# Kernel optimization log

Hardware: AMD Instinct MI355X
Metric: run time of the kernel (lower is better)

## Reference

```python
import jax, jax.numpy as jnp
import numpy as np

VOCAB = 9
D = 128      # EMBED_DIM
S = 64       # SEQ_LEN / context_length
B = 512      # batch
NH = 4       # num_heads
DH = D // NH # head dim = 32
NB = 2       # num_blocks
EPS = 1e-5


def setup_inputs() -> dict:
    key = jax.random.key(0)
    ks = jax.random.split(key, 10)
    rn = lambda k, shape: jax.random.normal(k, shape, jnp.float32) * 0.02
    return {
        "x": jax.random.randint(ks[0], (B, S), 0, VOCAB),
        "emb": rn(ks[1], (VOCAB, D)),
        "ln1_w": jnp.ones((NB, D), jnp.float32),          # pre-sLSTM LayerNorm weight
        "Wg": rn(ks[2], (NB, 4, NH, DH, DH)),             # headwise gate projections (i,f,z,o)
        "R": rn(ks[3], (NB, NH, DH, 4 * DH)),             # recurrent kernels per head
        "bias": rn(ks[4], (NB, NH, 4, DH)),               # cell bias per head/gate
        "gn_w": jnp.ones((NB, D), jnp.float32),           # multi-head (group) norm weight
        "ln2_w": jnp.ones((NB, D), jnp.float32),          # pre-FF LayerNorm weight
        "ff_up_w": rn(ks[5], (NB, 2 * D, D)),             # gated FF up projection
        "ff_down_w": rn(ks[6], (NB, D, D)),               # FF down projection
        "post_w": jnp.ones((D,), jnp.float32),            # post-blocks LayerNorm weight
        "proj_w": rn(ks[7], (VOCAB, D)),
        "proj_b": jnp.zeros((VOCAB,), jnp.float32),
    }


def _layernorm(x, w):
    mu = x.mean(-1, keepdims=True)
    var = x.var(-1, keepdims=True)
    return (x - mu) * jax.lax.rsqrt(var + EPS) * w


def _mh_groupnorm(h, w):
    # h: [B,S,NH,DH] -> normalize over DH per head, scale by per-channel w [D]
    mu = h.mean(-1, keepdims=True)
    var = h.var(-1, keepdims=True)
    hn = (h - mu) * jax.lax.rsqrt(var + EPS)
    return hn.reshape(h.shape[0], h.shape[1], D) * w


def _slstm_layer(xh, Wg, R, b):
    # xh: [B,S,NH,DH]; Wg: [4,NH,DH,DH]; R: [NH,DH,4*DH]; b: [NH,4,DH]
    gx = jnp.einsum('bsnh,gnkh->sbngk', xh, Wg)  # [S,B,NH,4,DH] gate preacts (i,f,z,o)

    def step(carry, g):
        h, c, n, m = carry  # each [B,NH,DH]
        ry = jnp.einsum('bnh,nhk->bnk', h, R).reshape(h.shape[0], NH, 4, DH)
        raw = g + ry + b
        i_r, f_r, z_r, o_r = raw[:, :, 0], raw[:, :, 1], raw[:, :, 2], raw[:, :, 3]
        logfplusm = m + jax.nn.log_sigmoid(f_r)
        mnew = jnp.maximum(i_r, logfplusm)            # stabilizer
        ig = jnp.exp(i_r - mnew)
        fg = jnp.exp(logfplusm - mnew)
        cnew = fg * c + ig * jnp.tanh(z_r)
        nnew = fg * n + ig
        hnew = jax.nn.sigmoid(o_r) * cnew / nnew
        return (hnew, cnew, nnew, mnew), hnew

    z0 = jnp.zeros((xh.shape[0], NH, DH), xh.dtype)
    _, hs = jax.lax.scan(step, (z0, z0, z0, z0), gx)
    return hs.transpose(1, 0, 2, 3)  # [B,S,NH,DH]


def reference(x, emb, ln1_w, Wg, R, bias, gn_w, ln2_w, ff_up_w, ff_down_w, post_w, proj_w, proj_b):
    h = emb[x]  # [B,S,D]
    for bi in range(NB):
        xn = _layernorm(h, ln1_w[bi])
        y = _slstm_layer(xn.reshape(h.shape[0], S, NH, DH), Wg[bi], R[bi], bias[bi])
        h = h + _mh_groupnorm(y, gn_w[bi])
        xn = _layernorm(h, ln2_w[bi])
        up = xn @ ff_up_w[bi].T                       # [B,S,2D]
        gate, upv = up[..., :D], up[..., D:]
        h = h + (jax.nn.gelu(gate, approximate=False) * upv) @ ff_down_w[bi].T
    h = _layernorm(h, post_w)
    return h @ proj_w.T + proj_b  # [B,S,VOCAB]
```

## Files before the change

### kernel.cpp

```cpp
#include <hip/hip_runtime.h>
#include <math.h>

#define D      128
#define S_LEN  64
#define B_SZ   512
#define NH     4
#define DH     32
#define NB     2
#define VOCAB  9
#define EPS    1e-5f
#define NTOK   (B_SZ * S_LEN)

template <int CTRL>
__device__ __forceinline__ float dppf(float x) {
    return __int_as_float(__builtin_amdgcn_update_dpp(
        0, __float_as_int(x), CTRL, 0xF, 0xF, true));
}
__device__ __forceinline__ float wsum64(float x) {
    x += dppf<0x111>(x);
    x += dppf<0x112>(x);
    x += dppf<0x114>(x);
    x += dppf<0x118>(x);
    x += dppf<0x142>(x);
    x += dppf<0x143>(x);
    return __int_as_float(__builtin_amdgcn_readlane(__float_as_int(x), 63));
}

__device__ __forceinline__ int xc3(int t, int c) { return c ^ (((t >> 1) & 7) << 2); }
__device__ __forceinline__ int xa (int t, int c) { return c ^ ((t & 7) << 2); }
__device__ __forceinline__ int xg (int c)        { return c ^ ((c >> 5) << 3); }

__global__ __launch_bounds__(256) void k_embed(const int* __restrict__ x,
                                               const float* __restrict__ emb,
                                               float* __restrict__ h,
                                               float* __restrict__ stats)
{
    int lane = threadIdx.x & 63;
    int wv   = threadIdx.x >> 6;
    int tok  = blockIdx.x * 4 + wv;
    int xi   = x[tok];
    float2 v = ((const float2*)(emb + xi * D))[lane];
    ((float2*)(h + (size_t)tok * D))[lane] = v;
    float s1 = wsum64(v.x + v.y);
    float s2 = wsum64(v.x * v.x + v.y * v.y);
    float mu  = s1 * (1.0f / D);
    float var = s2 * (1.0f / D) - mu * mu;
    if (lane == 0) {
        stats[tok * 2]     = mu;
        stats[tok * 2 + 1] = rsqrtf(var + EPS);
    }
}

__global__ __launch_bounds__(256, 2) void k_gx(const float* __restrict__ Wg,
                                               const float* __restrict__ bias,
                                               const float* __restrict__ lnw,
                                               const float* __restrict__ h,
                                               const float* __restrict__ stats,
                                               float* __restrict__ gx)
{
    __shared__ float xs[32 * 128];
    __shared__ float wl[4 * 32 * 128];

    int tid  = threadIdx.x;
    int lane = tid & 63;
    int wv   = tid >> 6;
    size_t tok0 = (size_t)blockIdx.x * 32;

    {
        int q = tid & 7;
        #pragma unroll
        for (int it = 0; it < 16; ++it) {
            int row = it * 32 + (tid >> 3);
            int g  = row >> 7;
            int n  = (row >> 5) & 3;
            int hh = row & 31;
            float4 v = *(const float4*)(Wg + row * 32 + q * 4);
            int col = g * 32 + hh;
            int sw  = q << 2;
            float* dst = wl + n * 4096;
            dst[(q * 4 + 0) * 128 + (col ^ sw)] = v.x;
            dst[(q * 4 + 1) * 128 + (col ^ sw)] = v.y;
            dst[(q * 4 + 2) * 128 + (col ^ sw)] = v.z;
            dst[(q * 4 + 3) * 128 + (col ^ sw)] = v.w;
        }
    }
    for (int i = 0; i < 8; ++i) {
        int t = wv * 8 + i;
        const float* hp = h + (tok0 + t) * D;
        float mu = stats[(tok0 + t) * 2];
        float rs = stats[(tok0 + t) * 2 + 1];
        float v1 = (hp[lane]      - mu) * rs * lnw[lane];
        float v2 = (hp[64 + lane] - mu) * rs * lnw[64 + lane];
        xs[t * 128 + xg(lane)]      = v1;
        xs[t * 128 + xg(lane + 64)] = v2;
    }
    __syncthreads();

    int nh   = lane >> 4;
    int col0 = (lane & 15) * 8;
    int t0   = wv * 8;

    float acc[8][8];
    #pragma unroll
    for (int j = 0; j < 8; ++j)
        #pragma unroll
        for (int cc = 0; cc < 8; ++cc) acc[j][cc] = 0.f;

    const float* wbase = wl + nh * 4096;
    #pragma unroll 4
    for (int k = 0; k < 32; ++k) {
        int sw = (k >> 2) << 2;
        float4 w0 = *(const float4*)&wbase[k * 128 + (col0 ^ sw)];
        float4 w1 = *(const float4*)&wbase[k * 128 + ((col0 + 4) ^ sw)];
        int ac = (nh * 32 + k) ^ (nh << 3);
        #pragma unroll
        for (int j = 0; j < 8; ++j) {
            float a = xs[(t0 + j) * 128 + ac];
            acc[j][0] = fmaf(a, w0.x, acc[j][0]);
            acc[j][1] = fmaf(a, w0.y, acc[j][1]);
            acc[j][2] = fmaf(a, w0.z, acc[j][2]);
            acc[j][3] = fmaf(a, w0.w, acc[j][3]);
            acc[j][4] = fmaf(a, w1.x, acc[j][4]);
            acc[j][5] = fmaf(a, w1.y, acc[j][5]);
            acc[j][6] = fmaf(a, w1.z, acc[j][6]);
            acc[j][7] = fmaf(a, w1.w, acc[j][7]);
        }
    }

    float4 bb0 = *(const float4*)(bias + nh * 128 + col0);
    float4 bb1 = *(const float4*)(bias + nh * 128 + col0 + 4);
    #pragma unroll
    for (int j = 0; j < 8; ++j) {
        int gt = (int)tok0 + t0 + j;
        int bb = gt >> 6;
        int ss = gt & 63;
        float* op = gx + ((size_t)(bb * NH + nh) * S_LEN + ss) * 128 + col0;
        float4 o0v, o1v;
        o0v.x = acc[j][0] + bb0.x; o0v.y = acc[j][1] + bb0.y;
        o0v.z = acc[j][2] + bb0.z; o0v.w = acc[j][3] + bb0.w;
        o1v.x = acc[j][4] + bb1.x; o1v.y = acc[j][5] + bb1.y;
        o1v.z = acc[j][6] + bb1.z; o1v.w = acc[j][7] + bb1.w;
        *(float4*)op       = o0v;
        *(float4*)(op + 4) = o1v;
    }
}

__global__ __launch_bounds__(64, 1) void k_scan(const float* __restrict__ Rm,
                                                const float* __restrict__ gnw,
                                                const float* __restrict__ gx,
                                                float* __restrict__ h)
{
    __shared__ float WA[8][64][4];
    __shared__ float WB[8][64][4];

    int b    = blockIdx.x >> 2;
    int n    = blockIdx.x & 3;
    int lane = threadIdx.x;
    int e    = lane >> 1;
    int sub  = lane & 1;
    int colA = sub * DH + e;

    #pragma unroll
    for (int cc = 0; cc < 8; ++cc) {
        float4 a, bv;
        #pragma unroll
        for (int j = 0; j < 4; ++j) {
            ((float*)&a)[j]  = Rm[(n * DH + cc * 4 + j) * 128 + colA];
            ((float*)&bv)[j] = Rm[(n * DH + cc * 4 + j) * 128 + 64 + colA];
        }
        *(float4*)WA[cc][lane] = a;
        *(float4*)WB[cc][lane] = bv;
    }
    float gw = gnw[n * DH + e];
    __syncthreads();

    float c = 0.f, nacc = 0.f, m = 0.f;
    float hu[DH];
    #pragma unroll
    for (int i = 0; i < DH; ++i) hu[i] = 0.f;

    float* hb = h + ((size_t)b * S_LEN) * D + n * DH;
    const float* gxp = gx + ((size_t)(b * NH + n) * S_LEN) * 128;

    float pGA[4], pGB[4], pHR[4];
    #pragma unroll
    for (int k = 0; k < 4; ++k) {
        pGA[k] = gxp[k * 128 + colA];
        pGB[k] = gxp[k * 128 + 64 + colA];
        pHR[k] = hb[k * D + e];
    }

    #pragma unroll 4
    for (int s = 0; s < S_LEN; ++s) {
        int sp = (s + 4 < S_LEN) ? s + 4 : S_LEN - 1;
        float nGA = gxp[sp * 128 + colA];
        float nGB = gxp[sp * 128 + 64 + colA];
        float nHR = hb[sp * D + e];

        float r0=0,r1=0,r2=0,r3=0,q0=0,q1=0,q2=0,q3=0;
        #pragma unroll
        for (int cc = 0; cc < 8; ++cc) {
            float4 wa = *(const float4*)WA[cc][lane];
            float4 wb = *(const float4*)WB[cc][lane];
            r0 = fmaf(hu[cc*4+0], wa.x, r0);
            r1 = fmaf(hu[cc*4+1], wa.y, r1);
            r2 = fmaf(hu[cc*4+2], wa.z, r2);
            r3 = fmaf(hu[cc*4+3], wa.w, r3);
            q0 = fmaf(hu[cc*4+0], wb.x, q0);
            q1 = fmaf(hu[cc*4+1], wb.y, q1);
            q2 = fmaf(hu[cc*4+2], wb.z, q2);
            q3 = fmaf(hu[cc*4+3], wb.w, q3);
        }
        float rawA = pGA[0] + ((r0 + r1) + (r2 + r3));
        float rawB = pGB[0] + ((q0 + q1) + (q2 + q3));

        float xA = dppf<0xB1>(rawA);
        float xB = dppf<0xB1>(rawB);
        float i_r = sub ? xA   : rawA;
        float f_r = sub ? rawA : xA;
        float z_r = sub ? xB   : rawB;
        float o_r = sub ? rawB : xB;

        float lsf  = fminf(f_r, 0.f)
                   - 0.69314718055994531f * __log2f(1.0f + __expf(-fabsf(f_r)));
        float lfm  = m + lsf;
        float mnew = fmaxf(i_r, lfm);
        float ig   = __expf(i_r - mnew);
        float fg   = __expf(lfm - mnew);
        float t    = __expf(2.f * z_r);
        float tz   = 1.f - 2.f / (t + 1.f);
        c    = fg * c + ig * tz;
        nacc = fg * nacc + ig;
        m    = mnew;
        float hv = c / (nacc * (1.f + __expf(-o_r)));

        float s1 = wsum64(hv);
        float s2 = wsum64(hv * hv);
        float mu  = s1 * (1.f / 64.f);
        float var = s2 * (1.f / 64.f) - mu * mu;
        float hn  = (hv - mu) * rsqrtf(var + EPS) * gw;

        if (!sub) hb[s * D + e] = pHR[0] + hn;

        #pragma unroll
        for (int i = 0; i < DH; ++i)
            hu[i] = __int_as_float(
                __builtin_amdgcn_readlane(__float_as_int(hv), 2 * i));

        pGA[0]=pGA[1]; pGA[1]=pGA[2]; pGA[2]=pGA[3]; pGA[3]=nGA;
        pGB[0]=pGB[1]; pGB[1]=pGB[2]; pGB[2]=pGB[3]; pGB[3]=nGB;
        pHR[0]=pHR[1]; pHR[1]=pHR[2]; pHR[2]=pHR[3]; pHR[3]=nHR;
    }
}

template <int LAST>
__global__ __launch_bounds__(256, 2) void k_ff(float* __restrict__ h,
                                               const float* __restrict__ ln2w,
                                               const float* __restrict__ wup,
                                               const float* __restrict__ wdn,
                                               float* __restrict__ stats_out,
                                               const float* __restrict__ lastw,
                                               const float* __restrict__ projw,
                                               const float* __restrict__ projb,
                                               float* __restrict__ out)
{
    __shared__ float xs[32 * 128];
    __shared__ float as_[32 * 64];
    __shared__ float wt[2 * 32 * 64];

    int tid  = threadIdx.x;
    int lane = tid & 63;
    int wv   = tid >> 6;
    size_t tok0 = (size_t)blockIdx.x * 32;

    for (int i = 0; i < 8; ++i) {
        int t = wv * 8 + i;
        const float* hp = h + (tok0 + t) * D;
        float v1 = hp[lane], v2 = hp[64 + lane];
        float s1 = wsum64(v1 + v2);
        float s2 = wsum64(v1 * v1 + v2 * v2);
        float mu = s1 * (1.0f / D);
        float rs = rsqrtf(s2 * (1.0f / D) - mu * mu + EPS);
        xs[t * D + xc3(t, lane)]      = (v1 - mu) * rs * ln2w[lane];
        xs[t * D + xc3(t, lane + 64)] = (v2 - mu) * rs * ln2w[64 + lane];
    }

    int q     = tid & 7;
    int r0    = tid >> 3;
    int goff0 = r0 * D + q * 4;
    int goff1 = (r0 + 32) * D + q * 4;
    int s0    = r0 ^ (q << 2);
    int kb    = q * 4;

    auto ffld = [&](int id, float4* pre) {
        int p = (id >= 6) ? 1 : 0;
        int j = id - p * 6;
        const float* b0;
        const float* b1;
        if (j < 4) { b0 = wup + (p * 64) * D + j * 32;
                     b1 = wup + (128 + p * 64) * D + j * 32; }
        else       { int jj = j - 4;
                     b0 = wdn + p * 64 + jj * 32;
                     b1 = wdn + 64 * D + p * 64 + jj * 32; }
        pre[0] = *(const float4*)(b0 + goff0);
        pre[1] = *(const float4*)(b0 + goff1);
        pre[2] = *(const float4*)(b1 + goff0);
        pre[3] = *(const float4*)(b1 + goff1);
    };
    auto fst = [&](const float4* pre) {
        #pragma unroll
        for (int cc = 0; cc < 4; ++cc) {
            const float* p0 = (const float*)&pre[0];
            const float* p1 = (const float*)&pre[1];
            const float* p2 = (const float*)&pre[2];
            const float* p3 = (const float*)&pre[3];
            wt[(kb + cc) * 64 + s0]           = p0[cc];
            wt[(kb + cc) * 64 + s0 + 32]      = p1[cc];
            wt[2048 + (kb + cc) * 64 + s0]      = p2[cc];
            wt[2048 + (kb + cc) * 64 + s0 + 32] = p3[cc];
        }
    };

    int ti = tid >> 4;
    int oi = tid & 15;
    int t0 = ti * 2;
    int o0 = oi * 4;

    float accd[2][2][4];
    #pragma unroll
    for (int a1 = 0; a1 < 2; ++a1)
        #pragma unroll
        for (int j = 0; j < 2; ++j)
            #pragma unroll
            for (int cc = 0; cc < 4; ++cc) accd[a1][j][cc] = 0.f;

    float4 pre[4];
    ffld(0, pre);
    int id = 1;

    #pragma unroll
    for (int p = 0; p < 2; ++p) {
        float accg[2][4], accv[2][4];
        #pragma unroll
        for (int j = 0; j < 2; ++j)
            #pragma unroll
            for (int cc = 0; cc < 4; ++cc) { accg[j][cc] = 0.f; accv[j][cc] = 0.f; }

        for (int c4 = 0; c4 < 4; ++c4) {
            __syncthreads();
            fst(pre);
            if (id < 12) ffld(id, pre);
            ++id;
            __syncthreads();
            int kc = c4 * 32;
            #pragma unroll
            for (int k4 = 0; k4 < 8; ++k4) {
                float4 a0 = *(const float4*)&xs[t0 * D + xc3(t0, kc + k4 * 4)];
                float4 a1v = *(const float4*)&xs[(t0 + 1) * D + xc3(t0 + 1, kc + k4 * 4)];
                int ws = k4 << 2;
                #pragma unroll
                for (int i = 0; i < 4; ++i) {
                    int k = k4 * 4 + i;
                    float4 bg = *(const float4*)&wt[k * 64 + (o0 ^ ws)];
                    float4 bv = *(const float4*)&wt[2048 + k * 64 + (o0 ^ ws)];
                    float ax0 = ((const float*)&a0)[i];
                    float ax1 = ((const float*)&a1v)[i];
                    accg[0][0] = fmaf(ax0, bg.x, accg[0][0]);
                    accg[0][1] = fmaf(ax0, bg.y, accg[0][1]);
                    accg[0][2] = fmaf(ax0, bg.z, accg[0][2]);
                    accg[0][3] = fmaf(ax0, bg.w, accg[0][3]);
                    accg[1][0] = fmaf(ax1, bg.x, accg[1][0]);
                    accg[1][1] = fmaf(ax1, bg.y, accg[1][1]);
                    accg[1][2] = fmaf(ax1, bg.z, accg[1][2]);
                    accg[1][3] = fmaf(ax1, bg.w, accg[1][3]);
                    accv[0][0] = fmaf(ax0, bv.x, accv[0][0]);
                    accv[0][1] = fmaf(ax0, bv.y, accv[0][1]);
                    accv[0][2] = fmaf(ax0, bv.z, accv[0][2]);
                    accv[0][3] = fmaf(ax0, bv.w, accv[0][3]);
                    accv[1][0] = fmaf(ax1, bv.x, accv[1][0]);
                    accv[1][1] = fmaf(ax1, bv.y, accv[1][1]);
                    accv[1][2] = fmaf(ax1, bv.z, accv[1][2]);
                    accv[1][3] = fmaf(ax1, bv.w, accv[1][3]);
                }
            }
        }
        #pragma unroll
        for (int j = 0; j < 2; ++j) {
            int t = t0 + j;
            float4 av;
            float* ap = (float*)&av;
            #pragma unroll
            for (int cc = 0; cc < 4; ++cc) {
                float g = accg[j][cc];
                float u = accv[j][cc];
                ap[cc] = 0.5f * g * (1.0f + erff(g * 0.70710678118654752f)) * u;
            }
            *(float4*)&as_[t * 64 + xa(t, o0)] = av;
        }
        for (int c2 = 0; c2 < 2; ++c2) {
            __syncthreads();
            fst(pre);
            if (id < 12) ffld(id, pre);
            ++id;
            __syncthreads();
            int kc = c2 * 32;
            #pragma unroll
            for (int k4 = 0; k4 < 8; ++k4) {
                float4 a0 = *(const float4*)&as_[t0 * 64 + xa(t0, kc + k4 * 4)];
                float4 a1v = *(const float4*)&as_[(t0 + 1) * 64 + xa(t0 + 1, kc + k4 * 4)];
                int ws = k4 << 2;
                #pragma unroll
                for (int i = 0; i < 4; ++i) {
                    int k = k4 * 4 + i;
                    float4 b0v = *(const float4*)&wt[k * 64 + (o0 ^ ws)];
                    float4 b1v = *(const float4*)&wt[2048 + k * 64 + (o0 ^ ws)];
                    float ax0 = ((const float*)&a0)[i];
                    float ax1 = ((const float*)&a1v)[i];
                    accd[0][0][0] = fmaf(ax0, b0v.x, accd[0][0][0]);
                    accd[0][0][1] = fmaf(ax0, b0v.y, accd[0][0][1]);
                    accd[0][0][2] = fmaf(ax0, b0v.z, accd[0][0][2]);
                    accd[0][0][3] = fmaf(ax0, b0v.w, accd[0][0][3]);
                    accd[0][1][0] = fmaf(ax1, b0v.x, accd[0][1][0]);
                    accd[0][1][1] = fmaf(ax1, b0v.y, accd[0][1][1]);
                    accd[0][1][2] = fmaf(ax1, b0v.z, accd[0][1][2]);
                    accd[0][1][3] = fmaf(ax1, b0v.w, accd[0][1][3]);
                    accd[1][0][0] = fmaf(ax0, b1v.x, accd[1][0][0]);
                    accd[1][0][1] = fmaf(ax0, b1v.y, accd[1][0][1]);
                    accd[1][0][2] = fmaf(ax0, b1v.z, accd[1][0][2]);
                    accd[1][0][3] = fmaf(ax0, b1v.w, accd[1][0][3]);
                    accd[1][1][0] = fmaf(ax1, b1v.x, accd[1][1][0]);
                    accd[1][1][1] = fmaf(ax1, b1v.y, accd[1][1][1]);
                    accd[1][1][2] = fmaf(ax1, b1v.z, accd[1][1][2]);
                    accd[1][1][3] = fmaf(ax1, b1v.w, accd[1][1][3]);
                }
            }
        }
    }

    #pragma unroll
    for (int j = 0; j < 2; ++j) {
        int t = t0 + j;
        size_t tok = tok0 + t;
        #pragma unroll
        for (int a1 = 0; a1 < 2; ++a1) {
            int cb = a1 * 64 + o0;
            float4 hres = *(const float4*)(h + tok * D + cb);
            float4 hn;
            hn.x = hres.x + accd[a1][j][0];
            hn.y = hres.y + accd[a1][j][1];
            hn.z = hres.z + accd[a1][j][2];
            hn.w = hres.w + accd[a1][j][3];
            if (!LAST) *(float4*)(h + tok * D + cb) = hn;
            *(float4*)&xs[t * D + xc3(t, cb)] = hn;
        }
    }
    __syncthreads();

    if (!LAST) {
        for (int i = 0; i < 8; ++i) {
            int t = wv * 8 + i;
            float v1 = xs[t * D + xc3(t, lane)];
            float v2 = xs[t * D + xc3(t, lane + 64)];
            float s1 = wsum64(v1 + v2);
            float s2 = wsum64(v1 * v1 + v2 * v2);
            float mu = s1 * (1.0f / D);
            float rs = rsqrtf(s2 * (1.0f / D) - mu * mu + EPS);
            if (lane == 0) {
                stats_out[(tok0 + t) * 2]     = mu;
                stats_out[(tok0 + t) * 2 + 1] = rs;
            }
        }
    } else {
        float pw1[VOCAB], pw2[VOCAB], pb[VOCAB];
        #pragma unroll
        for (int v = 0; v < VOCAB; ++v) {
            pw1[v] = projw[v * D + lane];
            pw2[v] = projw[v * D + 64 + lane];
            pb[v]  = projb[v];
        }
        for (int i = 0; i < 8; ++i) {
            int t = wv * 8 + i;
            float v1 = xs[t * D + xc3(t, lane)];
            float v2 = xs[t * D + xc3(t, lane + 64)];
            float s1 = wsum64(v1 + v2);
            float s2 = wsum64(v1 * v1 + v2 * v2);
            float mu = s1 * (1.0f / D);
            float rs = rsqrtf(s2 * (1.0f / D) - mu * mu + EPS);
            float x1 = (v1 - mu) * rs * lastw[lane];
            float x2 = (v2 - mu) * rs * lastw[64 + lane];
            #pragma unroll
            for (int v = 0; v < VOCAB; ++v) {
                float pp = wsum64(fmaf(x1, pw1[v], x2 * pw2[v]));
                if (lane == 0) out[(tok0 + t) * VOCAB + v] = pp + pb[v];
            }
        }
    }
}

extern "C" void kernel_launch(void* const* d_in, const int* in_sizes, int n_in,
                              void* d_out, int out_size, void* d_ws, size_t ws_size,
                              hipStream_t stream)
{
    const int*   x     = (const int*)  d_in[0];
    const float* emb   = (const float*)d_in[1];
    const float* ln1   = (const float*)d_in[2];
    const float* Wg    = (const float*)d_in[3];
    const float* Rm    = (const float*)d_in[4];
    const float* bias  = (const float*)d_in[5];
    const float* gnw   = (const float*)d_in[6];
    const float* ln2   = (const float*)d_in[7];
    const float* wup   = (const float*)d_in[8];
    const float* wdn   = (const float*)d_in[9];
    const float* postw = (const float*)d_in[10];
    const float* projw = (const float*)d_in[11];
    const float* projb = (const float*)d_in[12];
    float* out   = (float*)d_out;
    float* hbuf  = (float*)d_ws;
    float* stats = hbuf + (size_t)NTOK * D;
    float* gxbuf = stats + (size_t)NTOK * 2;

    k_embed<<<NTOK / 4, 256, 0, stream>>>(x, emb, hbuf, stats);

    for (int bi = 0; bi < NB; ++bi) {
        k_gx<<<NTOK / 32, 256, 0, stream>>>(Wg + bi * 4 * NH * DH * DH,
                                            bias + bi * NH * 4 * DH,
                                            ln1 + bi * D,
                                            hbuf, stats, gxbuf);
        k_scan<<<B_SZ * NH, 64, 0, stream>>>(Rm + bi * NH * DH * 4 * DH,
                                             gnw + bi * D,
                                             gxbuf, hbuf);
        if (bi == 0)
            k_ff<0><<<NTOK / 32, 256, 0, stream>>>(hbuf, ln2 + bi * D,
                                                   wup + bi * 2 * D * D,
                                                   wdn + bi * D * D,
                                                   stats, nullptr, nullptr,
                                                   nullptr, nullptr);
        else
            k_ff<1><<<NTOK / 32, 256, 0, stream>>>(hbuf, ln2 + bi * D,
                                                   wup + bi * 2 * D * D,
                                                   wdn + bi * D * D,
                                                   nullptr, postw, projw,
                                                   projb, out);
    }
}
```

Baseline: 386.0 us.

## Split sLSTM scan gates across two wavefronts with LDS hidden-state exchange

The recurrent scan block now uses two wavefronts. One computes the i/f gates and the cell update, the other computes the z/o gates (tanh and the sigmoid denominator) and passes them through shared memory. Recurrent weights sit in registers instead of LDS, and the hidden state is broadcast through a double-buffered LDS array rather than 32 readlanes. This halves the per-wave FMA chain and allows more blocks per CU. In exchange it adds two block barriers per timestep on the serial critical path.

Measured after the change: 391.4 us. Within noise of the previous version (+1.4%).

```diff
diff --git a/kernel.cpp b/kernel.cpp
--- a/kernel.cpp
+++ b/kernel.cpp
@@ -145,111 +145,135 @@
     }
 }
 
-__global__ __launch_bounds__(64, 1) void k_scan(const float* __restrict__ Rm,
-                                                const float* __restrict__ gnw,
-                                                const float* __restrict__ gx,
-                                                float* __restrict__ h)
+__global__ __launch_bounds__(128, 4) void k_scan(const float* __restrict__ Rm,
+                                                 const float* __restrict__ gnw,
+                                                 const float* __restrict__ gx,
+                                                 float* __restrict__ h)
 {
-    __shared__ float WA[8][64][4];
-    __shared__ float WB[8][64][4];
+    __shared__ float hub[2][32];
+    __shared__ float2 ts[32];
 
     int b    = blockIdx.x >> 2;
     int n    = blockIdx.x & 3;
-    int lane = threadIdx.x;
+    int tid  = threadIdx.x;
+    int wv   = tid >> 6;
+    int lane = tid & 63;
     int e    = lane >> 1;
     int sub  = lane & 1;
     int colA = sub * DH + e;
 
-    #pragma unroll
-    for (int cc = 0; cc < 8; ++cc) {
-        float4 a, bv;
-        #pragma unroll
-        for (int j = 0; j < 4; ++j) {
-            ((float*)&a)[j]  = Rm[(n * DH + cc * 4 + j) * 128 + colA];
-            ((float*)&bv)[j] = Rm[(n * DH + cc * 4 + j) * 128 + 64 + colA];
-        }
-        *(float4*)WA[cc][lane] = a;
-        *(float4*)WB[cc][lane] = bv;
-    }
-    float gw = gnw[n * DH + e];
+    const float* gxp = gx + ((size_t)(b * NH + n) * S_LEN) * 128;
+    float* hb = h + ((size_t)b * S_LEN) * D + n * DH;
+
+    float4 wr[8];
+    {
+        int cb = wv * 64 + colA;
+        #pragma unroll
+        for (int cc = 0; cc < 8; ++cc)
+            #pragma unroll
+            for (int j = 0; j < 4; ++j)
+                ((float*)&wr[cc])[j] = Rm[(n * DH + cc * 4 + j) * 128 + cb];
+    }
+    if (tid < 32) hub[0][tid] = 0.f;
     __syncthreads();
 
-    float c = 0.f, nacc = 0.f, m = 0.f;
-    float hu[DH];
-    #pragma unroll
-    for (int i = 0; i < DH; ++i) hu[i] = 0.f;
-
-    float* hb = h + ((size_t)b * S_LEN) * D + n * DH;
-    const float* gxp = gx + ((size_t)(b * NH + n) * S_LEN) * 128;
-
-    float pGA[4], pGB[4], pHR[4];
-    #pragma unroll
-    for (int k = 0; k < 4; ++k) {
-        pGA[k] = gxp[k * 128 + colA];
-        pGB[k] = gxp[k * 128 + 64 + colA];
-        pHR[k] = hb[k * D + e];
-    }
-
-    #pragma unroll 4
-    for (int s = 0; s < S_LEN; ++s) {
-        int sp = (s + 4 < S_LEN) ? s + 4 : S_LEN - 1;
-        float nGA = gxp[sp * 128 + colA];
-        float nGB = gxp[sp * 128 + 64 + colA];
-        float nHR = hb[sp * D + e];
-
-        float r0=0,r1=0,r2=0,r3=0,q0=0,q1=0,q2=0,q3=0;
-        #pragma unroll
-        for (int cc = 0; cc < 8; ++cc) {
-            float4 wa = *(const float4*)WA[cc][lane];
-            float4 wb = *(const float4*)WB[cc][lane];
-            r0 = fmaf(hu[cc*4+0], wa.x, r0);
-            r1 = fmaf(hu[cc*4+1], wa.y, r1);
-            r2 = fmaf(hu[cc*4+2], wa.z, r2);
-            r3 = fmaf(hu[cc*4+3], wa.w, r3);
-            q0 = fmaf(hu[cc*4+0], wb.x, q0);
-            q1 = fmaf(hu[cc*4+1], wb.y, q1);
-            q2 = fmaf(hu[cc*4+2], wb.z, q2);
-            q3 = fmaf(hu[cc*4+3], wb.w, q3);
-        }
-        float rawA = pGA[0] + ((r0 + r1) + (r2 + r3));
-        float rawB = pGB[0] + ((q0 + q1) + (q2 + q3));
-
-        float xA = dppf<0xB1>(rawA);
-        float xB = dppf<0xB1>(rawB);
-        float i_r = sub ? xA   : rawA;
-        float f_r = sub ? rawA : xA;
-        float z_r = sub ? xB   : rawB;
-        float o_r = sub ? rawB : xB;
-
-        float lsf  = fminf(f_r, 0.f)
-                   - 0.69314718055994531f * __log2f(1.0f + __expf(-fabsf(f_r)));
-        float lfm  = m + lsf;
-        float mnew = fmaxf(i_r, lfm);
-        float ig   = __expf(i_r - mnew);
-        float fg   = __expf(lfm - mnew);
-        float t    = __expf(2.f * z_r);
-        float tz   = 1.f - 2.f / (t + 1.f);
-        c    = fg * c + ig * tz;
-        nacc = fg * nacc + ig;
-        m    = mnew;
-        float hv = c / (nacc * (1.f + __expf(-o_r)));
-
-        float s1 = wsum64(hv);
-        float s2 = wsum64(hv * hv);
-        float mu  = s1 * (1.f / 64.f);
-        float var = s2 * (1.f / 64.f) - mu * mu;
-        float hn  = (hv - mu) * rsqrtf(var + EPS) * gw;
-
-        if (!sub) hb[s * D + e] = pHR[0] + hn;
-
-        #pragma unroll
-        for (int i = 0; i < DH; ++i)
-            hu[i] = __int_as_float(
-                __builtin_amdgcn_readlane(__float_as_int(hv), 2 * i));
-
-        pGA[0]=pGA[1]; pGA[1]=pGA[2]; pGA[2]=pGA[3]; pGA[3]=nGA;
-        pGB[0]=pGB[1]; pGB[1]=pGB[2]; pGB[2]=pGB[3]; pGB[3]=nGB;
-        pHR[0]=pHR[1]; pHR[1]=pHR[2]; pHR[2]=pHR[3]; pHR[3]=nHR;
+    if (wv == 0) {
+        float gw = gnw[n * DH + e];
+        float c = 0.f, nacc = 0.f, m = 0.f;
+        float pGA[4], pHR[4];
+        #pragma unroll
+        for (int k = 0; k < 4; ++k) {
+            pGA[k] = gxp[k * 128 + colA];
+            pHR[k] = hb[k * D + e];
+        }
+        int p = 0;
+        for (int s = 0; s < S_LEN; ++s) {
+            int sp = (s + 4 < S_LEN) ? s + 4 : S_LEN - 1;
+            float nGA = gxp[sp * 128 + colA];
+            float nHR = hb[sp * D + e];
+
+            float4 hv4[8];
+            #pragma unroll
+            for (int i = 0; i < 8; ++i) hv4[i] = ((const float4*)hub[p])[i];
+            float r0=0,r1=0,r2=0,r3=0;
+            #pragma unroll
+            for (int cc = 0; cc < 8; ++cc) {
+                r0 = fmaf(hv4[cc].x, wr[cc].x, r0);
+                r1 = fmaf(hv4[cc].y, wr[cc].y, r1);
+                r2 = fmaf(hv4[cc].z, wr[cc].z, r2);
+                r3 = fmaf(hv4[cc].w, wr[cc].w, r3);
+            }
+            float rawA = pGA[0] + ((r0 + r1) + (r2 + r3));
+
+            float xA = dppf<0xB1>(rawA);
+            float i_r = sub ? xA   : rawA;
+            float f_r = sub ? rawA : xA;
+
+            float lsf  = fminf(f_r, 0.f)
+                       - 0.69314718055994531f * __log2f(1.0f + __expf(-fabsf(f_r)));
+            float lfm  = m + lsf;
+            float mnew = fmaxf(i_r, lfm);
+            float ig   = __expf(i_r - mnew);
+            float fg   = __expf(lfm - mnew);
+            nacc = fg * nacc + ig;
+            m    = mnew;
+
+            __syncthreads();
+            float2 t2 = ts[e];
+            c = fg * c + ig * t2.x;
+            float hv = c / (nacc * t2.y);
+
+            float s1 = wsum64(hv);
+            float s2 = wsum64(hv * hv);
+            float mu  = s1 * (1.f / 64.f);
+            float var = s2 * (1.f / 64.f) - mu * mu;
+            float hn  = (hv - mu) * rsqrtf(var + EPS) * gw;
+
+            if (!sub) {
+                hb[s * D + e]  = pHR[0] + hn;
+                hub[p ^ 1][e]  = hv;
+            }
+            __syncthreads();
+            p ^= 1;
+            pGA[0]=pGA[1]; pGA[1]=pGA[2]; pGA[2]=pGA[3]; pGA[3]=nGA;
+            pHR[0]=pHR[1]; pHR[1]=pHR[2]; pHR[2]=pHR[3]; pHR[3]=nHR;
+        }
+    } else {
+        float pGB[4];
+        #pragma unroll
+        for (int k = 0; k < 4; ++k)
+            pGB[k] = gxp[k * 128 + 64 + colA];
+        int p = 0;
+        for (int s = 0; s < S_LEN; ++s) {
+            int sp = (s + 4 < S_LEN) ? s + 4 : S_LEN - 1;
+            float nGB = gxp[sp * 128 + 64 + colA];
+
+            float4 hv4[8];
+            #pragma unroll
+            for (int i = 0; i < 8; ++i) hv4[i] = ((const float4*)hub[p])[i];
+            float r0=0,r1=0,r2=0,r3=0;
+            #pragma unroll
+            for (int cc = 0; cc < 8; ++cc) {
+                r0 = fmaf(hv4[cc].x, wr[cc].x, r0);
+                r1 = fmaf(hv4[cc].y, wr[cc].y, r1);
+                r2 = fmaf(hv4[cc].z, wr[cc].z, r2);
+                r3 = fmaf(hv4[cc].w, wr[cc].w, r3);
+            }
+            float rawB = pGB[0] + ((r0 + r1) + (r2 + r3));
+
+            float xB = dppf<0xB1>(rawB);
+            float zz = sub ? xB   : rawB;
+            float oo = sub ? rawB : xB;
+            float arg = sub ? -oo : 2.f * zz;
+            float ee  = __expf(arg);
+            float res = sub ? (1.f + ee) : (1.f - 2.f / (ee + 1.f));
+            ((float*)ts)[2 * e + sub] = res;
+
+            __syncthreads();
+            __syncthreads();
+            p ^= 1;
+            pGB[0]=pGB[1]; pGB[1]=pGB[2]; pGB[2]=pGB[3]; pGB[3]=nGB;
+        }
     }
 }
 
@@ -526,9 +550,9 @@
                                             bias + bi * NH * 4 * DH,
                                             ln1 + bi * D,
                                             hbuf, stats, gxbuf);
-        k_scan<<<B_SZ * NH, 64, 0, stream>>>(Rm + bi * NH * DH * 4 * DH,
-                                             gnw + bi * D,
-                                             gxbuf, hbuf);
+        k_scan<<<B_SZ * NH, 128, 0, stream>>>(Rm + bi * NH * DH * 4 * DH,
+                                              gnw + bi * D,
+                                              gxbuf, hbuf);
         if (bi == 0)
             k_ff<0><<<NTOK / 32, 256, 0, stream>>>(hbuf, ln2 + bi * D,
                                                    wup + bi * 2 * D * D,
```

## Fuse gate projection into sLSTM scan kernel, keeping weights in registers

Applied to the files above, without the earlier changes.

Removes the separate k_gx kernel and the gx intermediate buffer. Each scan workgroup now normalizes its own 64 tokens into LDS and computes the headwise gate preactivations one chunk ahead, using Wg rows held in registers. The recurrent weights also move from LDS into registers. This removes a large global write and read of gx plus one launch per block, at the cost of extra register pressure and gate-projection math on the serial scan path.

After: 354.7 us (median of 3 runs). 8.1% less time.

```diff
diff --git a/kernel.cpp b/kernel.cpp
--- a/kernel.cpp
+++ b/kernel.cpp
@@ -28,7 +28,14 @@
 
 __device__ __forceinline__ int xc3(int t, int c) { return c ^ (((t >> 1) & 7) << 2); }
 __device__ __forceinline__ int xa (int t, int c) { return c ^ ((t & 7) << 2); }
-__device__ __forceinline__ int xg (int c)        { return c ^ ((c >> 5) << 3); }
+
+__device__ __forceinline__ float dot4(float4 a, float4 b, float c) {
+    c = fmaf(a.x, b.x, c);
+    c = fmaf(a.y, b.y, c);
+    c = fmaf(a.z, b.z, c);
+    c = fmaf(a.w, b.w, c);
+    return c;
+}
 
 __global__ __launch_bounds__(256) void k_embed(const int* __restrict__ x,
                                                const float* __restrict__ emb,
@@ -51,107 +58,16 @@
     }
 }
 
-__global__ __launch_bounds__(256, 2) void k_gx(const float* __restrict__ Wg,
-                                               const float* __restrict__ bias,
-                                               const float* __restrict__ lnw,
-                                               const float* __restrict__ h,
-                                               const float* __restrict__ stats,
-                                               float* __restrict__ gx)
+__global__ __launch_bounds__(64, 2) void k_gxscan(
+    const float* __restrict__ Wg,
+    const float* __restrict__ Rm,
+    const float* __restrict__ bias,
+    const float* __restrict__ lnw,
+    const float* __restrict__ gnw,
+    const float* __restrict__ stats,
+    float* __restrict__ h)
 {
-    __shared__ float xs[32 * 128];
-    __shared__ float wl[4 * 32 * 128];
-
-    int tid  = threadIdx.x;
-    int lane = tid & 63;
-    int wv   = tid >> 6;
-    size_t tok0 = (size_t)blockIdx.x * 32;
-
-    {
-        int q = tid & 7;
-        #pragma unroll
-        for (int it = 0; it < 16; ++it) {
-            int row = it * 32 + (tid >> 3);
-            int g  = row >> 7;
-            int n  = (row >> 5) & 3;
-            int hh = row & 31;
-            float4 v = *(const float4*)(Wg + row * 32 + q * 4);
-            int col = g * 32 + hh;
-            int sw  = q << 2;
-            float* dst = wl + n * 4096;
-            dst[(q * 4 + 0) * 128 + (col ^ sw)] = v.x;
-            dst[(q * 4 + 1) * 128 + (col ^ sw)] = v.y;
-            dst[(q * 4 + 2) * 128 + (col ^ sw)] = v.z;
-            dst[(q * 4 + 3) * 128 + (col ^ sw)] = v.w;
-        }
-    }
-    for (int i = 0; i < 8; ++i) {
-        int t = wv * 8 + i;
-        const float* hp = h + (tok0 + t) * D;
-        float mu = stats[(tok0 + t) * 2];
-        float rs = stats[(tok0 + t) * 2 + 1];
-        float v1 = (hp[lane]      - mu) * rs * lnw[lane];
-        float v2 = (hp[64 + lane] - mu) * rs * lnw[64 + lane];
-        xs[t * 128 + xg(lane)]      = v1;
-        xs[t * 128 + xg(lane + 64)] = v2;
-    }
-    __syncthreads();
-
-    int nh   = lane >> 4;
-    int col0 = (lane & 15) * 8;
-    int t0   = wv * 8;
-
-    float acc[8][8];
-    #pragma unroll
-    for (int j = 0; j < 8; ++j)
-        #pragma unroll
-        for (int cc = 0; cc < 8; ++cc) acc[j][cc] = 0.f;
-
-    const float* wbase = wl + nh * 4096;
-    #pragma unroll 4
-    for (int k = 0; k < 32; ++k) {
-        int sw = (k >> 2) << 2;
-        float4 w0 = *(const float4*)&wbase[k * 128 + (col0 ^ sw)];
-        float4 w1 = *(const float4*)&wbase[k * 128 + ((col0 + 4) ^ sw)];
-        int ac = (nh * 32 + k) ^ (nh << 3);
-        #pragma unroll
-        for (int j = 0; j < 8; ++j) {
-            float a = xs[(t0 + j) * 128 + ac];
-            acc[j][0] = fmaf(a, w0.x, acc[j][0]);
-            acc[j][1] = fmaf(a, w0.y, acc[j][1]);
-            acc[j][2] = fmaf(a, w0.z, acc[j][2]);
-            acc[j][3] = fmaf(a, w0.w, acc[j][3]);
-            acc[j][4] = fmaf(a, w1.x, acc[j][4]);
-            acc[j][5] = fmaf(a, w1.y, acc[j][5]);
-            acc[j][6] = fmaf(a, w1.z, acc[j][6]);
-            acc[j][7] = fmaf(a, w1.w, acc[j][7]);
-        }
-    }
-
-    float4 bb0 = *(const float4*)(bias + nh * 128 + col0);
-    float4 bb1 = *(const float4*)(bias + nh * 128 + col0 + 4);
-    #pragma unroll
-    for (int j = 0; j < 8; ++j) {
-        int gt = (int)tok0 + t0 + j;
-        int bb = gt >> 6;
-        int ss = gt & 63;
-        float* op = gx + ((size_t)(bb * NH + nh) * S_LEN + ss) * 128 + col0;
-        float4 o0v, o1v;
-        o0v.x = acc[j][0] + bb0.x; o0v.y = acc[j][1] + bb0.y;
-        o0v.z = acc[j][2] + bb0.z; o0v.w = acc[j][3] + bb0.w;
-        o1v.x = acc[j][4] + bb1.x; o1v.y = acc[j][5] + bb1.y;
-        o1v.z = acc[j][6] + bb1.z; o1v.w = acc[j][7] + bb1.w;
-        *(float4*)op       = o0v;
-        *(float4*)(op + 4) = o1v;
-    }
-}
-
-__global__ __launch_bounds__(64, 1) void k_scan(const float* __restrict__ Rm,
-                                                const float* __restrict__ gnw,
-                                                const float* __restrict__ gx,
-                                                float* __restrict__ h)
-{
-    __shared__ float WA[8][64][4];
-    __shared__ float WB[8][64][4];
+    __shared__ float xl[64 * 32];
 
     int b    = blockIdx.x >> 2;
     int n    = blockIdx.x & 3;
@@ -160,96 +76,133 @@
     int sub  = lane & 1;
     int colA = sub * DH + e;
 
+    size_t tok0 = (size_t)b * S_LEN;
+
+    {
+        const float* hrow = h + (tok0 + lane) * D + n * DH;
+        float2 st = ((const float2*)stats)[tok0 + lane];
+        float mu = st.x, rs = st.y;
+        #pragma unroll
+        for (int q = 0; q < 8; ++q) {
+            float4 v = *(const float4*)(hrow + q * 4);
+            float4 o;
+            o.x = (v.x - mu) * rs * lnw[n * DH + q * 4 + 0];
+            o.y = (v.y - mu) * rs * lnw[n * DH + q * 4 + 1];
+            o.z = (v.z - mu) * rs * lnw[n * DH + q * 4 + 2];
+            o.w = (v.w - mu) * rs * lnw[n * DH + q * 4 + 3];
+            *(float4*)&xl[lane * 32 + ((q ^ (lane & 7)) << 2)] = o;
+        }
+    }
+    __syncthreads();
+
+    int gA = sub;
+    int gB = 2 + sub;
+    const float* wrowA = Wg + ((size_t)(gA * NH + n) * DH + e) * DH;
+    const float* wrowB = Wg + ((size_t)(gB * NH + n) * DH + e) * DH;
+    float4 wgA[8], wgB[8], wrA[8], wrB[8];
     #pragma unroll
     for (int cc = 0; cc < 8; ++cc) {
-        float4 a, bv;
+        wgA[cc] = *(const float4*)(wrowA + cc * 4);
+        wgB[cc] = *(const float4*)(wrowB + cc * 4);
         #pragma unroll
         for (int j = 0; j < 4; ++j) {
-            ((float*)&a)[j]  = Rm[(n * DH + cc * 4 + j) * 128 + colA];
-            ((float*)&bv)[j] = Rm[(n * DH + cc * 4 + j) * 128 + 64 + colA];
-        }
-        *(float4*)WA[cc][lane] = a;
-        *(float4*)WB[cc][lane] = bv;
-    }
-    float gw = gnw[n * DH + e];
-    __syncthreads();
-
+            ((float*)&wrA[cc])[j] = Rm[(n * DH + cc * 4 + j) * 128 + colA];
+            ((float*)&wrB[cc])[j] = Rm[(n * DH + cc * 4 + j) * 128 + 64 + colA];
+        }
+    }
+    float biasA = bias[(n * 4 + gA) * DH + e];
+    float biasB = bias[(n * 4 + gB) * DH + e];
+    float gw    = gnw[n * DH + e];
+
+    auto gxpair = [&](int s, float& ga, float& gb) {
+        float a0 = 0.f, a1 = 0.f, b0 = 0.f, b1 = 0.f;
+        #pragma unroll
+        for (int cc = 0; cc < 8; cc += 2) {
+            float4 x0 = *(const float4*)&xl[s * 32 + ((cc ^ (s & 7)) << 2)];
+            float4 x1 = *(const float4*)&xl[s * 32 + (((cc + 1) ^ (s & 7)) << 2)];
+            a0 = dot4(x0, wgA[cc],     a0);
+            a1 = dot4(x1, wgA[cc + 1], a1);
+            b0 = dot4(x0, wgB[cc],     b0);
+            b1 = dot4(x1, wgB[cc + 1], b1);
+        }
+        ga = biasA + (a0 + a1);
+        gb = biasB + (b0 + b1);
+    };
+
+    float curA[8], curB[8], nxtA[8], nxtB[8];
+    #pragma unroll
+    for (int i = 0; i < 8; ++i) gxpair(i, curA[i], curB[i]);
+
+    float hu[32];
+    #pragma unroll
+    for (int i = 0; i < 32; ++i) hu[i] = 0.f;
     float c = 0.f, nacc = 0.f, m = 0.f;
-    float hu[DH];
-    #pragma unroll
-    for (int i = 0; i < DH; ++i) hu[i] = 0.f;
-
-    float* hb = h + ((size_t)b * S_LEN) * D + n * DH;
-    const float* gxp = gx + ((size_t)(b * NH + n) * S_LEN) * 128;
-
-    float pGA[4], pGB[4], pHR[4];
-    #pragma unroll
-    for (int k = 0; k < 4; ++k) {
-        pGA[k] = gxp[k * 128 + colA];
-        pGB[k] = gxp[k * 128 + 64 + colA];
-        pHR[k] = hb[k * D + e];
-    }
-
-    #pragma unroll 4
-    for (int s = 0; s < S_LEN; ++s) {
-        int sp = (s + 4 < S_LEN) ? s + 4 : S_LEN - 1;
-        float nGA = gxp[sp * 128 + colA];
-        float nGB = gxp[sp * 128 + 64 + colA];
-        float nHR = hb[sp * D + e];
-
-        float r0=0,r1=0,r2=0,r3=0,q0=0,q1=0,q2=0,q3=0;
-        #pragma unroll
-        for (int cc = 0; cc < 8; ++cc) {
-            float4 wa = *(const float4*)WA[cc][lane];
-            float4 wb = *(const float4*)WB[cc][lane];
-            r0 = fmaf(hu[cc*4+0], wa.x, r0);
-            r1 = fmaf(hu[cc*4+1], wa.y, r1);
-            r2 = fmaf(hu[cc*4+2], wa.z, r2);
-            r3 = fmaf(hu[cc*4+3], wa.w, r3);
-            q0 = fmaf(hu[cc*4+0], wb.x, q0);
-            q1 = fmaf(hu[cc*4+1], wb.y, q1);
-            q2 = fmaf(hu[cc*4+2], wb.z, q2);
-            q3 = fmaf(hu[cc*4+3], wb.w, q3);
-        }
-        float rawA = pGA[0] + ((r0 + r1) + (r2 + r3));
-        float rawB = pGB[0] + ((q0 + q1) + (q2 + q3));
-
-        float xA = dppf<0xB1>(rawA);
-        float xB = dppf<0xB1>(rawB);
-        float i_r = sub ? xA   : rawA;
-        float f_r = sub ? rawA : xA;
-        float z_r = sub ? xB   : rawB;
-        float o_r = sub ? rawB : xB;
-
-        float lsf  = fminf(f_r, 0.f)
-                   - 0.69314718055994531f * __log2f(1.0f + __expf(-fabsf(f_r)));
-        float lfm  = m + lsf;
-        float mnew = fmaxf(i_r, lfm);
-        float ig   = __expf(i_r - mnew);
-        float fg   = __expf(lfm - mnew);
-        float t    = __expf(2.f * z_r);
-        float tz   = 1.f - 2.f / (t + 1.f);
-        c    = fg * c + ig * tz;
-        nacc = fg * nacc + ig;
-        m    = mnew;
-        float hv = c / (nacc * (1.f + __expf(-o_r)));
-
-        float s1 = wsum64(hv);
-        float s2 = wsum64(hv * hv);
-        float mu  = s1 * (1.f / 64.f);
-        float var = s2 * (1.f / 64.f) - mu * mu;
-        float hn  = (hv - mu) * rsqrtf(var + EPS) * gw;
-
-        if (!sub) hb[s * D + e] = pHR[0] + hn;
-
-        #pragma unroll
-        for (int i = 0; i < DH; ++i)
-            hu[i] = __int_as_float(
-                __builtin_amdgcn_readlane(__float_as_int(hv), 2 * i));
-
-        pGA[0]=pGA[1]; pGA[1]=pGA[2]; pGA[2]=pGA[3]; pGA[3]=nGA;
-        pGB[0]=pGB[1]; pGB[1]=pGB[2]; pGB[2]=pGB[3]; pGB[3]=nGB;
-        pHR[0]=pHR[1]; pHR[1]=pHR[2]; pHR[2]=pHR[3]; pHR[3]=nHR;
+
+    float* hb = h + tok0 * D + n * DH;
+    float pHR[4];
+    #pragma unroll
+    for (int k = 0; k < 4; ++k) pHR[k] = hb[k * D + e];
+
+    for (int ch = 0; ch < 8; ++ch) {
+        #pragma unroll
+        for (int i = 0; i < 8; ++i) {
+            int s = ch * 8 + i;
+            if (ch < 7) gxpair(s + 8, nxtA[i], nxtB[i]);
+            int sp = (s + 4 < S_LEN) ? s + 4 : S_LEN - 1;
+            float nHR = hb[sp * D + e];
+
+            float r0=0,r1=0,r2=0,r3=0,q0=0,q1=0,q2=0,q3=0;
+            #pragma unroll
+            for (int cc = 0; cc < 8; ++cc) {
+                r0 = fmaf(hu[cc*4+0], wrA[cc].x, r0);
+                r1 = fmaf(hu[cc*4+1], wrA[cc].y, r1);
+                r2 = fmaf(hu[cc*4+2], wrA[cc].z, r2);
+                r3 = fmaf(hu[cc*4+3], wrA[cc].w, r3);
+                q0 = fmaf(hu[cc*4+0], wrB[cc].x, q0);
+                q1 = fmaf(hu[cc*4+1], wrB[cc].y, q1);
+                q2 = fmaf(hu[cc*4+2], wrB[cc].z, q2);
+                q3 = fmaf(hu[cc*4+3], wrB[cc].w, q3);
+            }
+            float rawA = curA[i] + ((r0 + r1) + (r2 + r3));
+            float rawB = curB[i] + ((q0 + q1) + (q2 + q3));
+
+            float xA = dppf<0xB1>(rawA);
+            float xB = dppf<0xB1>(rawB);
+            float i_r = sub ? xA   : rawA;
+            float f_r = sub ? rawA : xA;
+            float z_r = sub ? xB   : rawB;
+            float o_r = sub ? rawB : xB;
+
+            float lsf  = fminf(f_r, 0.f)
+                       - 0.69314718055994531f * __log2f(1.0f + __expf(-fabsf(f_r)));
+            float lfm  = m + lsf;
+            float mnew = fmaxf(i_r, lfm);
+            float ig   = __expf(i_r - mnew);
+            float fg   = __expf(lfm - mnew);
+            float t    = __expf(2.f * z_r);
+            float tz   = 1.f - 2.f / (t + 1.f);
+            c    = fg * c + ig * tz;
+            nacc = fg * nacc + ig;
+            m    = mnew;
+            float hv = c / (nacc * (1.f + __expf(-o_r)));
+
+            float s1 = wsum64(hv);
+            float s2 = wsum64(hv * hv);
+            float mu2 = s1 * (1.f / 64.f);
+            float var = s2 * (1.f / 64.f) - mu2 * mu2;
+            float hn  = (hv - mu2) * rsqrtf(var + EPS) * gw;
+
+            if (!sub) hb[s * D + e] = pHR[0] + hn;
+
+            #pragma unroll
+            for (int i2 = 0; i2 < 32; ++i2)
+                hu[i2] = __int_as_float(
+                    __builtin_amdgcn_readlane(__float_as_int(hv), 2 * i2));
+
+            pHR[0]=pHR[1]; pHR[1]=pHR[2]; pHR[2]=pHR[3]; pHR[3]=nHR;
+        }
+        #pragma unroll
+        for (int i = 0; i < 8; ++i) { curA[i] = nxtA[i]; curB[i] = nxtB[i]; }
     }
 }
 
@@ -517,18 +470,16 @@
     float* out   = (float*)d_out;
     float* hbuf  = (float*)d_ws;
     float* stats = hbuf + (size_t)NTOK * D;
-    float* gxbuf = stats + (size_t)NTOK * 2;
 
     k_embed<<<NTOK / 4, 256, 0, stream>>>(x, emb, hbuf, stats);
 
     for (int bi = 0; bi < NB; ++bi) {
-        k_gx<<<NTOK / 32, 256, 0, stream>>>(Wg + bi * 4 * NH * DH * DH,
-                                            bias + bi * NH * 4 * DH,
-                                            ln1 + bi * D,
-                                            hbuf, stats, gxbuf);
-        k_scan<<<B_SZ * NH, 64, 0, stream>>>(Rm + bi * NH * DH * 4 * DH,
-                                             gnw + bi * D,
-                                             gxbuf, hbuf);
+        k_gxscan<<<B_SZ * NH, 64, 0, stream>>>(Wg + bi * 4 * NH * DH * DH,
+                                               Rm + bi * NH * DH * 4 * DH,
+                                               bias + bi * NH * 4 * DH,
+                                               ln1 + bi * D,
+                                               gnw + bi * D,
+                                               stats, hbuf);
         if (bi == 0)
             k_ff<0><<<NTOK / 32, 256, 0, stream>>>(hbuf, ln2 + bi * D,
                                                    wup + bi * 2 * D * D,
```
